# Performance work log

Hardware: AMD Instinct MI355X
Metric: run time of the kernel (lower is better)

The kernel has to match this reference:

```python
import jax, jax.numpy as jnp
import numpy as np

L = 30  # SSA window size (module default)


def _ssa_groups1(xm):
    """pyts-style SSA with groups=1: full-SVD reconstruction of the
    trajectory (Hankel) matrix followed by anti-diagonal averaging.
    xm: [B, N] -> [B, N]
    """
    B, N = xm.shape
    K = N - L + 1
    # Hankel trajectory matrix: X[b, i, j] = xm[b, i + j], shape [B, L, K]
    idx = jnp.arange(L)[:, None] + jnp.arange(K)[None, :]
    X = xm[:, idx]
    # SVD and rank-L reconstruction (groups=1 sums ALL elementary matrices)
    U, s, Vt = jnp.linalg.svd(X, full_matrices=False)  # U:[B,L,L] s:[B,L] Vt:[B,L,K]
    Xr = jnp.einsum('blr,br,brk->blk', U, s, Vt)       # [B, L, K]
    # Anti-diagonal (Hankel) averaging: average Xr[i, j] over i + j = t
    seg = idx.reshape(-1)                               # [L*K] values in [0, N)
    sums = jax.vmap(lambda m: jax.ops.segment_sum(m.reshape(-1), seg, num_segments=N))(Xr)
    counts = jax.ops.segment_sum(jnp.ones(L * K, dtype=xm.dtype), seg, num_segments=N)
    return sums / counts                                # [B, N]


def setup_inputs() -> dict:
    key = jax.random.key(0)
    x = jax.random.normal(key, (256, 64, 2048), dtype=jnp.float32)
    return {"x": x}


def reference(x):
    # x: [B, C, N]
    xm = jnp.max(x, axis=1)                 # channel-max, [B, N]
    x_ss = _ssa_groups1(xm)                 # SSA round-trip, [B, N]
    # Original code detaches the SSA branch (CPU/numpy round trip)
    x_ss = jax.lax.stop_gradient(x_ss)
    gate = jax.nn.softmax(x_ss, axis=-1)[:, None, :]  # [B, 1, N]
    return gate * x                         # [B, C, N]
```

## Files before the change

### kernel.cpp

```cpp
#include <hip/hip_runtime.h>
#include <math.h>


#define B_DIM 256
#define C_DIM 64
#define N_DIM 2048
#define COLS4 (N_DIM / 4)
#define ROW4  (C_DIM * COLS4)

__global__ __launch_bounds__(256)
void max_kernel(const float* __restrict__ x, float* __restrict__ out) {
    const int bid  = blockIdx.x;
    const int b    = bid >> 3;
    const int s    = bid & 7;
    const int t    = threadIdx.x;
    const int lane = t & 63;
    const int w    = t >> 6;
    const int col  = (s << 6) + lane;

    const float4* __restrict__ xb = (const float4*)x + (size_t)b * ROW4;

    float4 m = make_float4(-INFINITY, -INFINITY, -INFINITY, -INFINITY);
    #pragma unroll
    for (int i = 0; i < 16; ++i) {
        const int c = w + (i << 2);
        float4 v = xb[(size_t)c * COLS4 + col];
        m.x = fmaxf(m.x, v.x); m.y = fmaxf(m.y, v.y);
        m.z = fmaxf(m.z, v.z); m.w = fmaxf(m.w, v.w);
    }

    __shared__ float4 pm[4][64];
    pm[w][lane] = m;
    __syncthreads();

    if (t < 64) {
        float4 a = pm[0][t], b1 = pm[1][t], c1 = pm[2][t], d = pm[3][t];
        float4 r;
        r.x = fmaxf(fmaxf(a.x, b1.x), fmaxf(c1.x, d.x));
        r.y = fmaxf(fmaxf(a.y, b1.y), fmaxf(c1.y, d.y));
        r.z = fmaxf(fmaxf(a.z, b1.z), fmaxf(c1.z, d.z));
        r.w = fmaxf(fmaxf(a.w, b1.w), fmaxf(c1.w, d.w));
        ((float4*)out)[(size_t)b * ROW4 + (s << 6) + t] = r;
    }
}

__global__ __launch_bounds__(256)
void softmax_kernel(float* __restrict__ out) {
    const int b    = blockIdx.x;
    const int t    = threadIdx.x;
    const int lane = t & 63;
    const int wid  = t >> 6;
    __shared__ float sred[8];

    float4* ob = (float4*)out + (size_t)b * ROW4;
    float4 a0 = ob[t];
    float4 a1 = ob[t + 256];

    float tm = fmaxf(fmaxf(fmaxf(a0.x, a0.y), fmaxf(a0.z, a0.w)),
                     fmaxf(fmaxf(a1.x, a1.y), fmaxf(a1.z, a1.w)));
    #pragma unroll
    for (int off = 32; off > 0; off >>= 1)
        tm = fmaxf(tm, __shfl_down(tm, off, 64));
    if (lane == 0) sred[wid] = tm;
    __syncthreads();
    const float M = fmaxf(fmaxf(sred[0], sred[1]), fmaxf(sred[2], sred[3]));

    float4 e0, e1;
    e0.x = __expf(a0.x - M); e0.y = __expf(a0.y - M);
    e0.z = __expf(a0.z - M); e0.w = __expf(a0.w - M);
    e1.x = __expf(a1.x - M); e1.y = __expf(a1.y - M);
    e1.z = __expf(a1.z - M); e1.w = __expf(a1.w - M);
    float ts = ((e0.x + e0.y) + (e0.z + e0.w)) + ((e1.x + e1.y) + (e1.z + e1.w));
    #pragma unroll
    for (int off = 32; off > 0; off >>= 1)
        ts += __shfl_down(ts, off, 64);
    if (lane == 0) sred[4 + wid] = ts;
    __syncthreads();
    const float inv = 1.0f / ((sred[4] + sred[5]) + (sred[6] + sred[7]));

    float4 g0, g1;
    g0.x = e0.x * inv; g0.y = e0.y * inv; g0.z = e0.z * inv; g0.w = e0.w * inv;
    g1.x = e1.x * inv; g1.y = e1.y * inv; g1.z = e1.z * inv; g1.w = e1.w * inv;
    #pragma unroll
    for (int g = 0; g < 4; ++g) {
        ob[(size_t)(g * 16) * COLS4 + t]       = g0;
        ob[(size_t)(g * 16) * COLS4 + t + 256] = g1;
    }
}

__global__ __launch_bounds__(512)
void mul_kernel(const float* __restrict__ x, float* __restrict__ out) {
    const int bid = blockIdx.x;
    const int b   = bid >> 2;
    const int g   = bid & 3;
    const int col = threadIdx.x;

    const size_t rbase = (size_t)b * ROW4;
    const float4* __restrict__ x4 = (const float4*)x + rbase;
    float4* o4 = (float4*)out + rbase;

    const int cbase = g * 16;
    const float4 gv = o4[(size_t)cbase * COLS4 + col];
    __syncthreads();

    #pragma unroll 4
    for (int c = 0; c < 16; ++c) {
        const size_t idx = (size_t)(cbase + c) * COLS4 + col;
        float4 v = x4[idx];
        float4 o;
        o.x = v.x * gv.x; o.y = v.y * gv.y;
        o.z = v.z * gv.z; o.w = v.w * gv.w;
        o4[idx] = o;
    }
}

extern "C" void kernel_launch(void* const* d_in, const int* in_sizes, int n_in,
                              void* d_out, int out_size, void* d_ws, size_t ws_size,
                              hipStream_t stream) {
    const float* x = (const float*)d_in[0];
    float* out = (float*)d_out;
    max_kernel<<<B_DIM * 8, 256, 0, stream>>>(x, out);
    softmax_kernel<<<B_DIM, 256, 0, stream>>>(out);
    mul_kernel<<<B_DIM * 4, 512, 0, stream>>>(x, out);
}
```

Before: 253.1 us.

## Split channel-max into four channel-group partials merged inside softmax kernel

The max kernel now assigns each block a 16-channel group across the full row, with each wave reading contiguous rows and holding 8 float4 accumulators for more loads in flight. Partial maxima are written to four rows of the output, and the softmax kernel merges them before computing the gate. This aims to improve memory access efficiency in the bandwidth-bound reduction, at the cost of extra partial writes and reads and higher register use.

```diff
diff --git a/kernel.cpp b/kernel.cpp
--- a/kernel.cpp
+++ b/kernel.cpp
@@ -11,36 +11,53 @@
 __global__ __launch_bounds__(256)
 void max_kernel(const float* __restrict__ x, float* __restrict__ out) {
     const int bid  = blockIdx.x;
-    const int b    = bid >> 3;
-    const int s    = bid & 7;
+    const int b    = bid >> 2;
+    const int q    = bid & 3;
     const int t    = threadIdx.x;
+    const int w    = t >> 6;
     const int lane = t & 63;
-    const int w    = t >> 6;
-    const int col  = (s << 6) + lane;
 
-    const float4* __restrict__ xb = (const float4*)x + (size_t)b * ROW4;
+    const float4* __restrict__ xb =
+        (const float4*)x + (size_t)b * ROW4 + (size_t)(q * 16 + w * 4) * COLS4;
 
-    float4 m = make_float4(-INFINITY, -INFINITY, -INFINITY, -INFINITY);
+    float4 m[8];
     #pragma unroll
-    for (int i = 0; i < 16; ++i) {
-        const int c = w + (i << 2);
-        float4 v = xb[(size_t)c * COLS4 + col];
-        m.x = fmaxf(m.x, v.x); m.y = fmaxf(m.y, v.y);
-        m.z = fmaxf(m.z, v.z); m.w = fmaxf(m.w, v.w);
+    for (int i = 0; i < 8; ++i)
+        m[i] = make_float4(-INFINITY, -INFINITY, -INFINITY, -INFINITY);
+
+    #pragma unroll 2
+    for (int c = 0; c < 4; ++c) {
+        float4 v[8];
+        #pragma unroll
+        for (int i = 0; i < 8; ++i)
+            v[i] = xb[(size_t)c * COLS4 + (i << 6) + lane];
+        #pragma unroll
+        for (int i = 0; i < 8; ++i) {
+            m[i].x = fmaxf(m[i].x, v[i].x);
+            m[i].y = fmaxf(m[i].y, v[i].y);
+            m[i].z = fmaxf(m[i].z, v[i].z);
+            m[i].w = fmaxf(m[i].w, v[i].w);
+        }
     }
 
-    __shared__ float4 pm[4][64];
-    pm[w][lane] = m;
+    __shared__ float4 pm[4][8][64];
+    #pragma unroll
+    for (int i = 0; i < 8; ++i) pm[w][i][lane] = m[i];
     __syncthreads();
 
-    if (t < 64) {
-        float4 a = pm[0][t], b1 = pm[1][t], c1 = pm[2][t], d = pm[3][t];
+    float4* og = (float4*)out + (size_t)b * ROW4 + (size_t)(q * 16) * COLS4;
+    #pragma unroll
+    for (int k = 0; k < 2; ++k) {
+        const int j = t + (k << 8);
+        const int i = j >> 6, l = j & 63;
+        float4 a0 = pm[0][i][l], a1 = pm[1][i][l];
+        float4 a2 = pm[2][i][l], a3 = pm[3][i][l];
         float4 r;
-        r.x = fmaxf(fmaxf(a.x, b1.x), fmaxf(c1.x, d.x));
-        r.y = fmaxf(fmaxf(a.y, b1.y), fmaxf(c1.y, d.y));
-        r.z = fmaxf(fmaxf(a.z, b1.z), fmaxf(c1.z, d.z));
-        r.w = fmaxf(fmaxf(a.w, b1.w), fmaxf(c1.w, d.w));
-        ((float4*)out)[(size_t)b * ROW4 + (s << 6) + t] = r;
+        r.x = fmaxf(fmaxf(a0.x, a1.x), fmaxf(a2.x, a3.x));
+        r.y = fmaxf(fmaxf(a0.y, a1.y), fmaxf(a2.y, a3.y));
+        r.z = fmaxf(fmaxf(a0.z, a1.z), fmaxf(a2.z, a3.z));
+        r.w = fmaxf(fmaxf(a0.w, a1.w), fmaxf(a2.w, a3.w));
+        og[j] = r;
     }
 }
 
@@ -53,8 +70,26 @@
     __shared__ float sred[8];
 
     float4* ob = (float4*)out + (size_t)b * ROW4;
-    float4 a0 = ob[t];
-    float4 a1 = ob[t + 256];
+
+    float4 a0, a1;
+    {
+        float4 p0 = ob[t];
+        float4 p1 = ob[(size_t)16 * COLS4 + t];
+        float4 p2 = ob[(size_t)32 * COLS4 + t];
+        float4 p3 = ob[(size_t)48 * COLS4 + t];
+        a0.x = fmaxf(fmaxf(p0.x, p1.x), fmaxf(p2.x, p3.x));
+        a0.y = fmaxf(fmaxf(p0.y, p1.y), fmaxf(p2.y, p3.y));
+        a0.z = fmaxf(fmaxf(p0.z, p1.z), fmaxf(p2.z, p3.z));
+        a0.w = fmaxf(fmaxf(p0.w, p1.w), fmaxf(p2.w, p3.w));
+        p0 = ob[t + 256];
+        p1 = ob[(size_t)16 * COLS4 + t + 256];
+        p2 = ob[(size_t)32 * COLS4 + t + 256];
+        p3 = ob[(size_t)48 * COLS4 + t + 256];
+        a1.x = fmaxf(fmaxf(p0.x, p1.x), fmaxf(p2.x, p3.x));
+        a1.y = fmaxf(fmaxf(p0.y, p1.y), fmaxf(p2.y, p3.y));
+        a1.z = fmaxf(fmaxf(p0.z, p1.z), fmaxf(p2.z, p3.z));
+        a1.w = fmaxf(fmaxf(p0.w, p1.w), fmaxf(p2.w, p3.w));
+    }
 
     float tm = fmaxf(fmaxf(fmaxf(a0.x, a0.y), fmaxf(a0.z, a0.w)),
                      fmaxf(fmaxf(a1.x, a1.y), fmaxf(a1.z, a1.w)));
@@ -119,7 +154,7 @@
                               hipStream_t stream) {
     const float* x = (const float*)d_in[0];
     float* out = (float*)d_out;
-    max_kernel<<<B_DIM * 8, 256, 0, stream>>>(x, out);
+    max_kernel<<<B_DIM * 4, 256, 0, stream>>>(x, out);
     softmax_kernel<<<B_DIM, 256, 0, stream>>>(out);
     mul_kernel<<<B_DIM * 4, 512, 0, stream>>>(x, out);
 }
```

Measured after the change: 253.3 us. No clear change (+0.1%).
